# Performance work log

Measured on AMD Instinct MI355X. Metric: run time of the kernel, lower is better.

Reference implementation:

```python
import jax, jax.numpy as jnp
import numpy as np

STRIDE = 4
HEADS = 8
KSIZE = 5
PAD_L = 4  # causal: kernel_size - 1


def _layernorm(x, g, b, eps=1e-5):
    mu = jnp.mean(x, axis=-1, keepdims=True)
    var = jnp.mean((x - mu) ** 2, axis=-1, keepdims=True)
    return (x - mu) * jax.lax.rsqrt(var + eps) * g + b


def setup_inputs() -> dict:
    key = jax.random.key(0)
    ks = jax.random.split(key, 6)
    B, T, C = 8, 2048, 1024
    D = 4096
    x = jax.random.normal(ks[0], (B, T, C), dtype=jnp.float32)
    W_proj = jax.random.normal(ks[1], (C * STRIDE, D), dtype=jnp.float32) * 0.02
    b_proj = jnp.zeros((D,), dtype=jnp.float32)
    ln_g = jnp.ones((D,), dtype=jnp.float32)
    ln_b = jnp.zeros((D,), dtype=jnp.float32)
    W_wgen = jax.random.normal(ks[2], (D, HEADS * KSIZE), dtype=jnp.float32) * 0.02
    b_wgen = jnp.zeros((HEADS * KSIZE,), dtype=jnp.float32)
    W_ff = jax.random.normal(ks[3], (D, D), dtype=jnp.float32) * 0.02
    b_ff = jnp.zeros((D,), dtype=jnp.float32)
    return {"x": x, "W_proj": W_proj, "b_proj": b_proj, "ln_g": ln_g, "ln_b": ln_b,
            "W_wgen": W_wgen, "b_wgen": b_wgen, "W_ff": W_ff, "b_ff": b_ff}


def reference(x, W_proj, b_proj, ln_g, ln_b, W_wgen, b_wgen, W_ff, b_ff):
    B, T, C = x.shape
    folded_T = T // STRIDE
    # fold time into channels, then dense projection to llm_dim
    xf = x[:, : folded_T * STRIDE].reshape(B, folded_T, C * STRIDE)
    h = xf @ W_proj + b_proj  # [B, Tf, D]
    D = h.shape[-1]
    R = D // HEADS
    # LConv1DBlock with norm_before + dynamic conv + (linear, relu, dropout p=0) + residual
    res = h
    y = _layernorm(h, ln_g, ln_b)
    # per-position dynamic weights, softmax over kernel taps
    w = (y @ W_wgen + b_wgen).reshape(B, folded_T, HEADS, KSIZE)
    w = jax.nn.softmax(w, axis=-1)  # [B, Tf, H, K]
    # causal depthwise conv: out[t] = sum_k w[t,k] * y[t - (K-1) + k]
    yp = jnp.pad(y, ((0, 0), (PAD_L, 0), (0, 0)))  # left pad time
    # stacked taps: [K, B, Tf, H, R]
    taps = jnp.stack([yp[:, k:k + folded_T] for k in range(KSIZE)], axis=0)
    taps = taps.reshape(KSIZE, B, folded_T, HEADS, R)
    conv = jnp.einsum('kbthr,bthk->bthr', taps, w).reshape(B, folded_T, D)
    # feed-forward ops: linear -> relu -> dropout(p=0)
    out = res + jax.nn.relu(conv @ W_ff + b_ff)
    return out
```

## Files before the change

### kernel.cpp

```cpp
#include <hip/hip_runtime.h>

typedef unsigned short u16;
typedef unsigned int u32;
typedef __attribute__((ext_vector_type(8))) short bf16x8;
typedef __attribute__((ext_vector_type(4))) float f32x4;

__device__ __forceinline__ float bf2f(u16 u) {
    union { u32 i; float f; } x; x.i = ((u32)u) << 16; return x.f;
}
__device__ __forceinline__ u16 f2bf(float f) {
    union { float f; u32 i; } x; x.f = f;
    u32 u = x.i;
    u += 0x7FFFu + ((u >> 16) & 1u);
    return (u16)(u >> 16);
}
__device__ __forceinline__ float wred(float v) {
    #pragma unroll
    for (int off = 32; off; off >>= 1) v += __shfl_down(v, off);
    return v;
}
__device__ __forceinline__ void gload_lds16(const void* g, void* l) {
    __builtin_amdgcn_global_load_lds(
        (const __attribute__((address_space(1))) u32*)g,
        (__attribute__((address_space(3))) u32*)l,
        16, 0, 0);
}

__global__ __launch_bounds__(256)
void cvt_f32_bf16(const float* __restrict__ in, u16* __restrict__ out) {
    int i = (blockIdx.x * 256 + threadIdx.x) * 4;
    float4 v = *(const float4*)(in + i);
    ushort4 p;
    p.x = f2bf(v.x); p.y = f2bf(v.y); p.z = f2bf(v.z); p.w = f2bf(v.w);
    *(ushort4*)(out + i) = p;
}

__global__ __launch_bounds__(256)
void transpose_cvt(const float* __restrict__ W, u16* __restrict__ Wt) {
    __shared__ float tile[64][65];
    int n0 = blockIdx.x * 64;
    int k0 = blockIdx.y * 64;
    int tx = threadIdx.x, ty = threadIdx.y;
    #pragma unroll
    for (int i = 0; i < 8; ++i) {
        int kk = ty + i * 8;
        const float* src = W + (size_t)(k0 + kk) * 4096 + n0;
        tile[kk][tx]      = src[tx];
        tile[kk][tx + 32] = src[tx + 32];
    }
    __syncthreads();
    #pragma unroll
    for (int i = 0; i < 8; ++i) {
        int nn = ty + i * 8;
        ushort2 p;
        p.x = f2bf(tile[tx * 2][nn]);
        p.y = f2bf(tile[tx * 2 + 1][nn]);
        *(ushort2*)(Wt + (size_t)(n0 + nn) * 4096 + k0 + tx * 2) = p;
    }
}

__global__ __launch_bounds__(256)
void transpose_wgen(const float* __restrict__ W, float* __restrict__ Wt) {
    int idx = blockIdx.x * 256 + threadIdx.x;
    int c = idx >> 12, e = idx & 4095;
    Wt[idx] = W[(size_t)e * 40 + c];
}

template <int MODE>
__global__ __launch_bounds__(512, 2)
void gemm256(const u16* __restrict__ A, const u16* __restrict__ Bt,
             const float* __restrict__ bias, const float* __restrict__ res,
             float* __restrict__ out) {
    const int K = 4096, N = 4096;
    __shared__ u16 smem[65536];

    const int tid = threadIdx.x;
    const int lane = tid & 63;
    const int w = tid >> 6;
    const int wr = w >> 2, wc = w & 3;
    const int fr = lane & 15;
    const int fk = (lane >> 4) * 8;
    const int cswz = (fr & 7) << 3;

    const int bid = blockIdx.x;
    const int swz = (bid & 7) * (gridDim.x >> 3) + (bid >> 3);
    const int tm = swz >> 4, tn = swz & 15;
    const size_t rowA0 = (size_t)tm * 256;
    const size_t rowB0 = (size_t)tn * 256;

    const int srl = lane >> 3;
    const int scl = ((lane & 7) ^ srl) << 3;

    f32x4 acc[8][4] = {};
    bf16x8 af[8];
    bf16x8 bh0[4];
    bf16x8 bh1[4];

    auto stA = [&](int b, int half, int kt) {
        #pragma unroll
        for (int i = 0; i < 2; ++i) {
            size_t grow = rowA0 + half * 128 + i * 64 + w * 8 + srl;
            gload_lds16(A + grow * K + kt * 64 + scl,
                        &smem[b * 32768 + half * 8192 + i * 4096 + w * 512 + lane * 8]);
        }
    };
    auto stB = [&](int b, int half, int kt) {
        #pragma unroll
        for (int i = 0; i < 2; ++i) {
            size_t grow = rowB0 + half * 128 + i * 64 + w * 8 + srl;
            gload_lds16(Bt + grow * K + kt * 64 + scl,
                        &smem[b * 32768 + 16384 + half * 8192 + i * 4096 + w * 512 + lane * 8]);
        }
    };
    auto ldA = [&](int b, int qm) {
        #pragma unroll
        for (int m = 0; m < 4; ++m) {
            int base = b * 32768 + (wr * 128 + (qm * 4 + m) * 16 + fr) * 64;
            af[m * 2 + 0] = *(const bf16x8*)&smem[base + (fk ^ cswz)];
            af[m * 2 + 1] = *(const bf16x8*)&smem[base + ((32 + fk) ^ cswz)];
        }
    };
    auto ldB = [&](int b, int qn, bf16x8 (&bh)[4]) {
        #pragma unroll
        for (int n = 0; n < 2; ++n) {
            int base = b * 32768 + 16384 + (wc * 64 + qn * 32 + n * 16 + fr) * 64;
            bh[n * 2 + 0] = *(const bf16x8*)&smem[base + (fk ^ cswz)];
            bh[n * 2 + 1] = *(const bf16x8*)&smem[base + ((32 + fk) ^ cswz)];
        }
    };
    auto mma = [&](int qm, int qn, bf16x8 (&bh)[4]) {
        __builtin_amdgcn_s_setprio(1);
        #pragma unroll
        for (int m = 0; m < 4; ++m)
            #pragma unroll
            for (int n = 0; n < 2; ++n) {
                acc[qm*4+m][qn*2+n] = __builtin_amdgcn_mfma_f32_16x16x32_bf16(
                    af[m*2+0], bh[n*2+0], acc[qm*4+m][qn*2+n], 0, 0, 0);
                acc[qm*4+m][qn*2+n] = __builtin_amdgcn_mfma_f32_16x16x32_bf16(
                    af[m*2+1], bh[n*2+1], acc[qm*4+m][qn*2+n], 0, 0, 0);
            }
        __builtin_amdgcn_s_setprio(0);
    };
    #define BAR() __builtin_amdgcn_s_barrier()
    #define VM4() asm volatile("s_waitcnt vmcnt(4)" ::: "memory")

    stB(0, 0, 0); stB(0, 1, 0); stA(0, 0, 0); stA(0, 1, 0);
    stB(1, 0, 1); stB(1, 1, 1);
    VM4();
    BAR();

    for (int i = 0; i < 32; ++i) {
        const int t = 2 * i;
        const int kt2 = (t + 2 < 64) ? t + 2 : 63;
        const int kt3 = (t + 3 < 64) ? t + 3 : 63;
        ldA(0, 0); ldB(0, 0, bh0);
        stA(1, 0, t + 1);
        BAR(); mma(0, 0, bh0);
        ldB(0, 1, bh1);
        stA(1, 1, t + 1);
        BAR(); mma(0, 1, bh1);
        ldA(0, 1);
        BAR(); mma(1, 1, bh1);
        stB(0, 0, kt2); stB(0, 1, kt2);
        VM4();
        BAR(); mma(1, 0, bh0);
        ldA(1, 0); ldB(1, 0, bh0);
        stA(0, 0, kt2);
        BAR(); mma(0, 0, bh0);
        ldB(1, 1, bh1);
        stA(0, 1, kt2);
        BAR(); mma(0, 1, bh1);
        ldA(1, 1);
        BAR(); mma(1, 1, bh1);
        stB(1, 0, kt3); stB(1, 1, kt3);
        VM4();
        BAR(); mma(1, 0, bh0);
    }
    #undef BAR
    #undef VM4

    const int cc = lane & 15;
    const int cr = (lane >> 4) * 4;
    #pragma unroll
    for (int m = 0; m < 8; ++m) {
        #pragma unroll
        for (int n = 0; n < 4; ++n) {
            size_t row = rowA0 + wr * 128 + m * 16 + cr;
            size_t col = rowB0 + wc * 64 + n * 16 + cc;
            float bv = bias[col];
            #pragma unroll
            for (int q = 0; q < 4; ++q) {
                size_t idx = (row + q) * (size_t)N + col;
                float v = acc[m][n][q] + bv;
                if (MODE == 1) v = res[idx] + fmaxf(v, 0.0f);
                out[idx] = v;
            }
        }
    }
}

__global__ __launch_bounds__(256)
void ln_wgen(const float* __restrict__ h, const float* __restrict__ g,
             const float* __restrict__ beta, const float* __restrict__ WgT,
             const float* __restrict__ bg, u16* __restrict__ y,
             float* __restrict__ w) {
    __shared__ u32 ylp[8][2048];
    __shared__ float red[8];
    __shared__ float wraw[8][40];

    int tid = threadIdx.x, lane = tid & 63, wv = tid >> 6;
    size_t row0 = (size_t)blockIdx.x * 8;

    for (int r = 0; r < 8; ++r) {
        const float4* hr = (const float4*)(h + (row0 + r) * 4096);
        float4 v[4];
        float s = 0.f, ss = 0.f;
        #pragma unroll
        for (int i = 0; i < 4; ++i) {
            v[i] = hr[tid + i * 256];
            s  += v[i].x + v[i].y + v[i].z + v[i].w;
            ss += v[i].x * v[i].x + v[i].y * v[i].y + v[i].z * v[i].z + v[i].w * v[i].w;
        }
        s = wred(s); ss = wred(ss);
        if (lane == 0) { red[wv] = s; red[4 + wv] = ss; }
        __syncthreads();
        float S = red[0] + red[1] + red[2] + red[3];
        float SS = red[4] + red[5] + red[6] + red[7];
        float mu = S * (1.0f / 4096.0f);
        float var = SS * (1.0f / 4096.0f) - mu * mu;
        float inv = rsqrtf(var + 1e-5f);
        u16* yr = y + (row0 + r) * 4096;
        #pragma unroll
        for (int i = 0; i < 4; ++i) {
            int base = tid + i * 256;
            float4 gv = ((const float4*)g)[base];
            float4 bv = ((const float4*)beta)[base];
            float o0 = (v[i].x - mu) * inv * gv.x + bv.x;
            float o1 = (v[i].y - mu) * inv * gv.y + bv.y;
            float o2 = (v[i].z - mu) * inv * gv.z + bv.z;
            float o3 = (v[i].w - mu) * inv * gv.w + bv.w;
            u32 p01 = (u32)f2bf(o0) | ((u32)f2bf(o1) << 16);
            u32 p23 = (u32)f2bf(o2) | ((u32)f2bf(o3) << 16);
            ylp[r][base * 2]     = p01;
            ylp[r][base * 2 + 1] = p23;
            uint2 pk; pk.x = p01; pk.y = p23;
            *(uint2*)(yr + base * 4) = pk;
        }
        __syncthreads();
    }

    float acc[8][10];
    #pragma unroll
    for (int r = 0; r < 8; ++r)
        #pragma unroll
        for (int c = 0; c < 10; ++c) acc[r][c] = 0.f;

    for (int eb = lane; eb < 2048; eb += 64) {
        float alo[8], ahi[8];
        #pragma unroll
        for (int r = 0; r < 8; ++r) {
            u32 a = ylp[r][eb];
            alo[r] = bf2f((u16)a);
            ahi[r] = bf2f((u16)(a >> 16));
        }
        #pragma unroll
        for (int c0 = 0; c0 < 10; ++c0) {
            int c = wv * 10 + c0;
            float2 wg = ((const float2*)(WgT + (size_t)c * 4096))[eb];
            #pragma unroll
            for (int r = 0; r < 8; ++r)
                acc[r][c0] += alo[r] * wg.x + ahi[r] * wg.y;
        }
    }
    #pragma unroll
    for (int r = 0; r < 8; ++r) {
        #pragma unroll
        for (int c0 = 0; c0 < 10; ++c0) {
            float p = wred(acc[r][c0]);
            if (lane == 0) wraw[r][wv * 10 + c0] = p + bg[wv * 10 + c0];
        }
    }
    __syncthreads();

    if (tid < 64) {
        int r = tid >> 3, hh = tid & 7;
        float e5[5];
        float mx = -1e30f;
        #pragma unroll
        for (int k = 0; k < 5; ++k) mx = fmaxf(mx, wraw[r][hh * 5 + k]);
        float sum = 0.f;
        #pragma unroll
        for (int k = 0; k < 5; ++k) { e5[k] = expf(wraw[r][hh * 5 + k] - mx); sum += e5[k]; }
        float isum = 1.0f / sum;
        float* wp = w + (row0 + r) * 40 + hh * 5;
        #pragma unroll
        for (int k = 0; k < 5; ++k) wp[k] = e5[k] * isum;
    }
}

__global__ __launch_bounds__(256)
void dconv2(const u16* __restrict__ y, const float* __restrict__ w,
            u16* __restrict__ conv) {
    int bid = blockIdx.x;
    int half = bid & 1;
    int rem = bid >> 1;
    int tc = rem % 18, b = rem / 18;
    int t0 = tc * 30;
    int d0 = half * 2048 + threadIdx.x * 8;
    int head = d0 >> 9;
    const u16* yb = y + (size_t)b * 512 * 4096 + d0;
    u16* cb = conv + (size_t)b * 512 * 4096 + d0;
    const float* wb = w + ((size_t)b * 512) * 40 + head * 5;

    float ring[5][8];
    #pragma unroll
    for (int j = 0; j < 4; ++j) {
        int tt = t0 - 4 + j;
        if (tt >= 0) {
            uint4 v = *(const uint4*)(yb + (size_t)tt * 4096);
            const u16* us = (const u16*)&v;
            #pragma unroll
            for (int e = 0; e < 8; ++e) ring[j + 1][e] = bf2f(us[e]);
        } else {
            #pragma unroll
            for (int e = 0; e < 8; ++e) ring[j + 1][e] = 0.f;
        }
    }

    for (int tt = 0; tt < 30; tt += 5) {
        #pragma unroll
        for (int j = 0; j < 5; ++j) {
            int t = t0 + tt + j;
            if (t < 512) {
                uint4 v = *(const uint4*)(yb + (size_t)t * 4096);
                const u16* us = (const u16*)&v;
                #pragma unroll
                for (int e = 0; e < 8; ++e) ring[j][e] = bf2f(us[e]);
                const float* wt = wb + (size_t)t * 40;
                float w0 = wt[0], w1 = wt[1], w2 = wt[2], w3 = wt[3], w4 = wt[4];
                u16 o[8];
                #pragma unroll
                for (int e = 0; e < 8; ++e) {
                    float a = w0 * ring[(j + 1) % 5][e]
                            + w1 * ring[(j + 2) % 5][e]
                            + w2 * ring[(j + 3) % 5][e]
                            + w3 * ring[(j + 4) % 5][e]
                            + w4 * ring[j][e];
                    o[e] = f2bf(a);
                }
                *(uint4*)(cb + (size_t)t * 4096) = *(uint4*)o;
            }
        }
    }
}

extern "C" void kernel_launch(void* const* d_in, const int* in_sizes, int n_in,
                              void* d_out, int out_size, void* d_ws, size_t ws_size,
                              hipStream_t stream) {
    const float* x      = (const float*)d_in[0];
    const float* W_proj = (const float*)d_in[1];
    const float* b_proj = (const float*)d_in[2];
    const float* ln_g   = (const float*)d_in[3];
    const float* ln_b   = (const float*)d_in[4];
    const float* W_wgen = (const float*)d_in[5];
    const float* b_wgen = (const float*)d_in[6];
    const float* W_ff   = (const float*)d_in[7];
    const float* b_ff   = (const float*)d_in[8];
    float* out = (float*)d_out;

    char* ws = (char*)d_ws;
    u16* xb   = (u16*)(ws);
    u16* WpT  = (u16*)(ws + ((size_t)32 << 20));
    u16* WfT  = (u16*)(ws + ((size_t)64 << 20));
    float* wbuf = (float*)(ws + ((size_t)96 << 20));
    float* WgT  = (float*)(ws + ((size_t)97 << 20));
    u16* conv = xb;
    u16* ybuf = WpT;

    cvt_f32_bf16<<<16384, 256, 0, stream>>>(x, xb);
    dim3 tb(32, 8);
    transpose_cvt<<<dim3(64, 64), tb, 0, stream>>>(W_proj, WpT);
    transpose_cvt<<<dim3(64, 64), tb, 0, stream>>>(W_ff, WfT);
    transpose_wgen<<<640, 256, 0, stream>>>(W_wgen, WgT);

    gemm256<0><<<256, 512, 0, stream>>>(xb, WpT, b_proj, nullptr, out);
    ln_wgen<<<512, 256, 0, stream>>>(out, ln_g, ln_b, WgT, b_wgen, ybuf, wbuf);
    dconv2<<<288, 256, 0, stream>>>(ybuf, wbuf, conv);
    gemm256<1><<<256, 512, 0, stream>>>(conv, WfT, b_ff, out, out);
}
```

Before: 359.2 us.

## Reorder MFMA k-loop, split B-tile stores across barriers, retile dynamic conv

Three unrelated changes. The GEMM inner MMA loop now issues all first-half-K MFMAs before the second half, so consecutive MFMAs do not hit the same accumulator back to back. The two global-to-LDS stores for the next B tile are split across a barrier so the memory traffic interleaves with compute. The depthwise conv kernel now uses 16-timestep chunks over 512 blocks instead of 30-step chunks over 288, with a fully unrolled shift-register window and no bounds check. This gives more parallelism, but each block redundantly reloads more halo rows.

```diff
diff --git a/kernel.cpp b/kernel.cpp
--- a/kernel.cpp
+++ b/kernel.cpp
@@ -131,14 +131,13 @@
     auto mma = [&](int qm, int qn, bf16x8 (&bh)[4]) {
         __builtin_amdgcn_s_setprio(1);
         #pragma unroll
-        for (int m = 0; m < 4; ++m)
+        for (int kk = 0; kk < 2; ++kk)
             #pragma unroll
-            for (int n = 0; n < 2; ++n) {
-                acc[qm*4+m][qn*2+n] = __builtin_amdgcn_mfma_f32_16x16x32_bf16(
-                    af[m*2+0], bh[n*2+0], acc[qm*4+m][qn*2+n], 0, 0, 0);
-                acc[qm*4+m][qn*2+n] = __builtin_amdgcn_mfma_f32_16x16x32_bf16(
-                    af[m*2+1], bh[n*2+1], acc[qm*4+m][qn*2+n], 0, 0, 0);
-            }
+            for (int m = 0; m < 4; ++m)
+                #pragma unroll
+                for (int n = 0; n < 2; ++n)
+                    acc[qm*4+m][qn*2+n] = __builtin_amdgcn_mfma_f32_16x16x32_bf16(
+                        af[m*2+kk], bh[n*2+kk], acc[qm*4+m][qn*2+n], 0, 0, 0);
         __builtin_amdgcn_s_setprio(0);
     };
     #define BAR() __builtin_amdgcn_s_barrier()
@@ -160,8 +159,9 @@
         stA(1, 1, t + 1);
         BAR(); mma(0, 1, bh1);
         ldA(0, 1);
+        stB(0, 0, kt2);
         BAR(); mma(1, 1, bh1);
-        stB(0, 0, kt2); stB(0, 1, kt2);
+        stB(0, 1, kt2);
         VM4();
         BAR(); mma(1, 0, bh0);
         ldA(1, 0); ldB(1, 0, bh0);
@@ -171,8 +171,9 @@
         stA(0, 1, kt2);
         BAR(); mma(0, 1, bh1);
         ldA(1, 1);
+        stB(1, 0, kt3);
         BAR(); mma(1, 1, bh1);
-        stB(1, 0, kt3); stB(1, 1, kt3);
+        stB(1, 1, kt3);
         VM4();
         BAR(); mma(1, 0, bh0);
     }
@@ -299,58 +300,57 @@
 }
 
 __global__ __launch_bounds__(256)
-void dconv2(const u16* __restrict__ y, const float* __restrict__ w,
+void dconv3(const u16* __restrict__ y, const float* __restrict__ w,
             u16* __restrict__ conv) {
     int bid = blockIdx.x;
     int half = bid & 1;
     int rem = bid >> 1;
-    int tc = rem % 18, b = rem / 18;
-    int t0 = tc * 30;
+    int tc = rem & 31, b = rem >> 5;
+    int t0 = tc * 16;
     int d0 = half * 2048 + threadIdx.x * 8;
     int head = d0 >> 9;
     const u16* yb = y + (size_t)b * 512 * 4096 + d0;
     u16* cb = conv + (size_t)b * 512 * 4096 + d0;
     const float* wb = w + ((size_t)b * 512) * 40 + head * 5;
 
-    float ring[5][8];
-    #pragma unroll
-    for (int j = 0; j < 4; ++j) {
-        int tt = t0 - 4 + j;
-        if (tt >= 0) {
-            uint4 v = *(const uint4*)(yb + (size_t)tt * 4096);
-            const u16* us = (const u16*)&v;
-            #pragma unroll
-            for (int e = 0; e < 8; ++e) ring[j + 1][e] = bf2f(us[e]);
-        } else {
-            #pragma unroll
-            for (int e = 0; e < 8; ++e) ring[j + 1][e] = 0.f;
-        }
-    }
-
-    for (int tt = 0; tt < 30; tt += 5) {
-        #pragma unroll
-        for (int j = 0; j < 5; ++j) {
-            int t = t0 + tt + j;
-            if (t < 512) {
-                uint4 v = *(const uint4*)(yb + (size_t)t * 4096);
+    float r0[8], r1[8], r2[8], r3[8], r4[8];
+    {
+        float* slots[4] = { r1, r2, r3, r4 };
+        #pragma unroll
+        for (int j = 0; j < 4; ++j) {
+            int tt = t0 - 4 + j;
+            if (tt >= 0) {
+                uint4 v = *(const uint4*)(yb + (size_t)tt * 4096);
                 const u16* us = (const u16*)&v;
                 #pragma unroll
-                for (int e = 0; e < 8; ++e) ring[j][e] = bf2f(us[e]);
-                const float* wt = wb + (size_t)t * 40;
-                float w0 = wt[0], w1 = wt[1], w2 = wt[2], w3 = wt[3], w4 = wt[4];
-                u16 o[8];
+                for (int e = 0; e < 8; ++e) slots[j][e] = bf2f(us[e]);
+            } else {
                 #pragma unroll
-                for (int e = 0; e < 8; ++e) {
-                    float a = w0 * ring[(j + 1) % 5][e]
-                            + w1 * ring[(j + 2) % 5][e]
-                            + w2 * ring[(j + 3) % 5][e]
-                            + w3 * ring[(j + 4) % 5][e]
-                            + w4 * ring[j][e];
-                    o[e] = f2bf(a);
-                }
-                *(uint4*)(cb + (size_t)t * 4096) = *(uint4*)o;
+                for (int e = 0; e < 8; ++e) slots[j][e] = 0.f;
             }
         }
+    }
+
+    #pragma unroll
+    for (int tt = 0; tt < 16; ++tt) {
+        int t = t0 + tt;
+        #pragma unroll
+        for (int e = 0; e < 8; ++e) {
+            r0[e] = r1[e]; r1[e] = r2[e]; r2[e] = r3[e]; r3[e] = r4[e];
+        }
+        uint4 v = *(const uint4*)(yb + (size_t)t * 4096);
+        const u16* us = (const u16*)&v;
+        #pragma unroll
+        for (int e = 0; e < 8; ++e) r4[e] = bf2f(us[e]);
+        const float* wt = wb + (size_t)t * 40;
+        float w0 = wt[0], w1 = wt[1], w2 = wt[2], w3 = wt[3], w4 = wt[4];
+        u16 o[8];
+        #pragma unroll
+        for (int e = 0; e < 8; ++e) {
+            float a = w0 * r0[e] + w1 * r1[e] + w2 * r2[e] + w3 * r3[e] + w4 * r4[e];
+            o[e] = f2bf(a);
+        }
+        *(uint4*)(cb + (size_t)t * 4096) = *(uint4*)o;
     }
 }
 
@@ -385,6 +385,6 @@
 
     gemm256<0><<<256, 512, 0, stream>>>(xb, WpT, b_proj, nullptr, out);
     ln_wgen<<<512, 256, 0, stream>>>(out, ln_g, ln_b, WgT, b_wgen, ybuf, wbuf);
-    dconv2<<<288, 256, 0, stream>>>(ybuf, wbuf, conv);
+    dconv3<<<512, 256, 0, stream>>>(ybuf, wbuf, conv);
     gemm256<1><<<256, 512, 0, stream>>>(conv, WfT, b_ff, out, out);
 }
```

After: 351.6 us. 1.02x faster.
